# Kernel tuning notes

Measured on AMD Instinct MI355X. Metric: run time of the kernel, lower is better.

Reference implementation:

```python
import jax, jax.numpy as jnp
import numpy as np

NUM_GROUPS = 8
INPUT_DIM = 1024
OUTPUT_DIM = 1024
TOKENS_PER_GROUP = 8192  # rows per group after reshape


def setup_inputs() -> dict:
    key = jax.random.key(0)
    kx, kw = jax.random.split(key)
    # x: [N*G, D_in] as fed to the torch module (it reshapes internally)
    x = jax.random.normal(kx, (TOKENS_PER_GROUP * NUM_GROUPS, INPUT_DIM), dtype=jnp.float32)
    # Stacked per-group Linear weights, torch layout [D_out, D_in] per group.
    # Xavier-normal gain=1: std = sqrt(2 / (fan_in + fan_out))
    std = np.sqrt(2.0 / (INPUT_DIM + OUTPUT_DIM)).astype(np.float32)
    W = jax.random.normal(kw, (NUM_GROUPS, OUTPUT_DIM, INPUT_DIM), dtype=jnp.float32) * std
    return {"x": x, "W": W}


def reference(x, W):
    # x: [N*G, D_in] -> [N, G, D_in]
    n = x.shape[0] // NUM_GROUPS
    xg = x.reshape(n, NUM_GROUPS, INPUT_DIM)
    # per-group linear: out[n,g,k] = sum_d xg[n,g,d] * W[g,k,d]
    out = jnp.einsum("ngd,gkd->ngk", xg, W)
    return out.reshape(-1, OUTPUT_DIM)
```

## Files before the change

### kernel.cpp

```cpp
#include <hip/hip_runtime.h>
#include <hip/hip_bf16.h>


namespace {

constexpr int NG   = 8;
constexpr int DIN  = 1024;
constexpr int DOUT = 1024;
constexpr int BM   = 256;
constexpr int BN   = 256;
constexpr int BK   = 64;
constexpr int NKT  = DIN / BK;
constexpr int ROWB = BK * 2;
constexpr int LDS_TILE  = BM * ROWB;
constexpr int LDS_BYTES = 4 * LDS_TILE;
constexpr int JTN  = DOUT / BN;
constexpr size_t WSB_BYTES = (size_t)NG * JTN * NKT * LDS_TILE;

typedef __attribute__((ext_vector_type(8))) short bf16x8;
typedef __attribute__((ext_vector_type(4))) float f32x4;

__device__ __forceinline__ uint2 pack_bf16x4(f32x4 v) {
  union { __hip_bfloat162 h2[2]; uint2 u; } p;
  p.h2[0] = __float22bfloat162_rn(make_float2(v.x, v.y));
  p.h2[1] = __float22bfloat162_rn(make_float2(v.z, v.w));
  return p.u;
}

__device__ __forceinline__ void glds16(const void* g, void* l) {
  __builtin_amdgcn_global_load_lds(
      (const __attribute__((address_space(1))) unsigned int*)g,
      (__attribute__((address_space(3))) unsigned int*)l, 16, 0, 0);
}

#define FENCE() asm volatile("" ::: "memory")
#define BAR()   do { FENCE(); __builtin_amdgcn_s_barrier(); FENCE(); } while (0)
#define LGKM0() asm volatile("s_waitcnt lgkmcnt(0)" ::: "memory")
#define VM0()   asm volatile("s_waitcnt vmcnt(0)" ::: "memory")
#define MFMA_(a, b, c) __builtin_amdgcn_mfma_f32_16x16x32_bf16((a), (b), (c), 0, 0, 0)

__global__ __launch_bounds__(256)
void cvt_w_kernel(const float* __restrict__ W, char* __restrict__ wsB) {
  const int q    = (int)blockIdx.x * 256 + (int)threadIdx.x;
  const int tile = q >> 13;
  const int q13  = q & 8191;
  const int r    = q13 >> 5;
  const int cp   = q13 & 31;
  const int g    = tile >> 6;
  const int jt   = (tile >> 4) & 3;
  const int kt   = tile & 15;

  const float2 s = *(const float2*)(
      W + ((size_t)(g * DOUT + jt * 256 + r)) * DIN + kt * 64 + 2 * cp);
  union { __hip_bfloat162 h; unsigned u; } pk;
  pk.h = __float22bfloat162_rn(make_float2(s.x, s.y));

  const int swz = (r & 7) << 4;
  const int dstByte = r * 128 + (((cp >> 2) * 16) ^ swz) + (cp & 3) * 4;
  *(unsigned*)(wsB + (size_t)tile * LDS_TILE + dstByte) = pk.u;
}

#define QPHASE(KS, MH, PRE, POST)                                              \
  do {                                                                         \
    const int cx_ = (KS) ? colx1 : colx0;                                      \
    bf16x8 af0 = *(const bf16x8*)(cA + aRow0 + ((MH)*4+0)*2048 + cx_);         \
    bf16x8 af1 = *(const bf16x8*)(cA + aRow0 + ((MH)*4+1)*2048 + cx_);         \
    bf16x8 af2 = *(const bf16x8*)(cA + aRow0 + ((MH)*4+2)*2048 + cx_);         \
    bf16x8 af3 = *(const bf16x8*)(cA + aRow0 + ((MH)*4+3)*2048 + cx_);         \
    PRE                                                                        \
    BAR();                                                                     \
    LGKM0();                                                                   \
    __builtin_amdgcn_sched_barrier(0);                                         \
    __builtin_amdgcn_s_setprio(1);                                             \
    _Pragma("unroll")                                                          \
    for (int n = 0; n < 4; ++n) {                                              \
      acc[(MH)*4+0][n] = MFMA_(af0, bfr[n], acc[(MH)*4+0][n]);                 \
      acc[(MH)*4+1][n] = MFMA_(af1, bfr[n], acc[(MH)*4+1][n]);                 \
      acc[(MH)*4+2][n] = MFMA_(af2, bfr[n], acc[(MH)*4+2][n]);                 \
      acc[(MH)*4+3][n] = MFMA_(af3, bfr[n], acc[(MH)*4+3][n]);                 \
    }                                                                          \
    __builtin_amdgcn_s_setprio(0);                                             \
    POST                                                                       \
    BAR();                                                                     \
  } while (0)

template <bool WSB>
__global__ __launch_bounds__(512, 2)
void grouped_gemm_8p(const float* __restrict__ X,
                     const float* __restrict__ W,
                     const char* __restrict__ wsB,
                     float* __restrict__ O) {
  extern __shared__ char smem[];
  char* const smA = smem;
  char* const smB = smem + 2 * LDS_TILE;

  const int bid = (int)blockIdx.x;
  const int swz = (bid & 7) * 128 + (bid >> 3);
  const int jt = swz & 3;
  const int it = (swz >> 2) & 31;
  const int g  = swz >> 7;

  const int n0 = it * BM;
  const int c0 = jt * BN;

  const int tid  = (int)threadIdx.x;
  const int lane = tid & 63;
  const int wid  = tid >> 6;
  const int wr   = wid >> 2;
  const int wc   = wid & 3;

  const int s_lane = tid & 15;
  const int s_row  = tid >> 4;

  const float* Ag = X + ((size_t)(n0 + s_row) * NG + g) * DIN + s_lane * 4;
  constexpr size_t ASTR = (size_t)32 * NG * DIN;

  const float* Bg = W + (size_t)g * DOUT * DIN + (size_t)(c0 + s_row) * DIN
                      + s_lane * 4;
  constexpr size_t BSTR = (size_t)32 * DIN;

  const char* BgT = wsB + ((size_t)(g * JTN + jt) * NKT) * LDS_TILE;
  const int bOff = tid * 16;

  const int wb0 = s_row * ROWB + ((s_lane * 8) ^ ((s_row & 7) << 4));

  const int fr = lane & 15;
  const int fq = lane >> 4;
  const int swzm  = (fr & 7) << 4;
  const int colx0 = (fq * 16) ^ swzm;
  const int colx1 = (64 + fq * 16) ^ swzm;
  const int aRow0 = (wr * 128 + fr) * ROWB;
  const int bRow0 = (wc * 64  + fr) * ROWB;

  f32x4 aS[8], bS[8];
  f32x4 acc[8][4];
#pragma unroll
  for (int m = 0; m < 8; ++m)
#pragma unroll
    for (int n = 0; n < 4; ++n) acc[m][n] = (f32x4){0.f, 0.f, 0.f, 0.f};

  if (WSB) {
#pragma unroll
    for (int p = 0; p < 4; ++p)
      glds16(BgT + bOff + p * 8192, smB + bOff + p * 8192);
  } else {
#pragma unroll
    for (int p = 0; p < 8; ++p) bS[p] = *(const f32x4*)(Bg + p * BSTR);
  }
#pragma unroll
  for (int p = 0; p < 8; ++p) aS[p] = *(const f32x4*)(Ag + p * ASTR);
#pragma unroll
  for (int p = 0; p < 8; ++p)
    *(uint2*)(smA + wb0 + p * 4096) = pack_bf16x4(aS[p]);
  if (!WSB) {
#pragma unroll
    for (int p = 0; p < 8; ++p)
      *(uint2*)(smB + wb0 + p * 4096) = pack_bf16x4(bS[p]);
  }
  VM0();
  LGKM0();
  BAR();

#pragma unroll 2
  for (int t = 0; t < NKT; ++t) {
    char* const cA = smA + (t & 1) * LDS_TILE;
    char* const cB = smB + (t & 1) * LDS_TILE;
    char* const nA = smA + ((t & 1) ^ 1) * LDS_TILE;
    char* const nB = smB + ((t & 1) ^ 1) * LDS_TILE;
    const bool stage = (t + 1) < NKT;

    bf16x8 bfr[4];
#pragma unroll
    for (int n = 0; n < 4; ++n)
      bfr[n] = *(const bf16x8*)(cB + bRow0 + n * 2048 + colx0);

    QPHASE(0, 0,
      { if (stage) {
          const float* An = Ag + (size_t)(t + 1) * BK;
          _Pragma("unroll")
          for (int p = 0; p < 8; ++p) aS[p] = *(const f32x4*)(An + p * ASTR);
          if (WSB) {
            const char* Bn = BgT + (size_t)(t + 1) * LDS_TILE;
            _Pragma("unroll")
            for (int p = 0; p < 4; ++p)
              glds16(Bn + bOff + p * 8192, nB + bOff + p * 8192);
          }
        } },
      { });

    QPHASE(0, 1,
      { if (!WSB && stage) {
          const float* Bn = Bg + (size_t)(t + 1) * BK;
          _Pragma("unroll")
          for (int p = 0; p < 8; ++p) bS[p] = *(const f32x4*)(Bn + p * BSTR);
        } },
      { });

    QPHASE(1, 0,
      { _Pragma("unroll")
        for (int n = 0; n < 4; ++n)
          bfr[n] = *(const bf16x8*)(cB + bRow0 + n * 2048 + colx1);
      },
      { if (stage) {
          _Pragma("unroll")
          for (int p = 0; p < 8; ++p)
            *(uint2*)(nA + wb0 + p * 4096) = pack_bf16x4(aS[p]);
        } });

    QPHASE(1, 1, { },
      { if (!WSB && stage) {
          _Pragma("unroll")
          for (int p = 0; p < 8; ++p)
            *(uint2*)(nB + wb0 + p * 4096) = pack_bf16x4(bS[p]);
        }
        LGKM0();
        if (WSB && stage) { VM0(); } });
  }

#pragma unroll
  for (int m = 0; m < 8; ++m) {
#pragma unroll
    for (int r = 0; r < 4; ++r) {
      const int row = wr * 128 + m * 16 + fq * 4 + r;
      float* orow = O + ((size_t)(n0 + row) * NG + g) * DOUT + c0 + wc * 64;
#pragma unroll
      for (int n = 0; n < 4; ++n) {
        orow[n * 16 + fr] = acc[m][n][r];
      }
    }
  }
}

}

extern "C" void kernel_launch(void* const* d_in, const int* in_sizes, int n_in,
                              void* d_out, int out_size, void* d_ws, size_t ws_size,
                              hipStream_t stream) {
  (void)n_in; (void)out_size;
  const float* X = (const float*)d_in[0];
  const float* W = (const float*)d_in[1];
  float* O = (float*)d_out;

  const int tokens_total = in_sizes[0] / DIN;
  const int ntok_per_g   = tokens_total / NG;
  const int grid = NG * (ntok_per_g / BM) * (DOUT / BN);

  if (ws_size >= WSB_BYTES) {
    const int cvt_grid = (int)(WSB_BYTES / 4 / 256);
    cvt_w_kernel<<<dim3(cvt_grid), dim3(256), 0, stream>>>(W, (char*)d_ws);
    (void)hipFuncSetAttribute((const void*)grouped_gemm_8p<true>,
                              hipFuncAttributeMaxDynamicSharedMemorySize,
                              LDS_BYTES);
    grouped_gemm_8p<true><<<dim3(grid), dim3(512), LDS_BYTES, stream>>>(
        X, W, (const char*)d_ws, O);
  } else {
    (void)hipFuncSetAttribute((const void*)grouped_gemm_8p<false>,
                              hipFuncAttributeMaxDynamicSharedMemorySize,
                              LDS_BYTES);
    grouped_gemm_8p<false><<<dim3(grid), dim3(512), LDS_BYTES, stream>>>(
        X, W, nullptr, O);
  }
}
```

Measured before the change: 239.1 us.

## Pre-convert X to swizzled bf16 tiles and run a pure async-load GEMM

Adds a pre-pass kernel that converts X from fp32 into bf16 tiles laid out and swizzled exactly as the LDS expects, stored in workspace. A new GEMM kernel then streams both A and B through direct global-to-LDS loads, with no in-kernel fp32 loading or conversion of X. The aim is to halve the A-operand bytes the GEMM reads and to drop conversion work from its main loop. The cost is an extra pass that reads all of X and writes a bf16 copy, plus a larger workspace requirement; the older path is kept as a fallback when the workspace is too small.

```diff
diff --git a/kernel.cpp b/kernel.cpp
--- a/kernel.cpp
+++ b/kernel.cpp
@@ -15,7 +15,10 @@
 constexpr int LDS_TILE  = BM * ROWB;
 constexpr int LDS_BYTES = 4 * LDS_TILE;
 constexpr int JTN  = DOUT / BN;
+constexpr int ITN  = 32;
 constexpr size_t WSB_BYTES = (size_t)NG * JTN * NKT * LDS_TILE;
+constexpr size_t WSA_BYTES = (size_t)NG * ITN * NKT * LDS_TILE;
+constexpr size_t WSF_BYTES = WSA_BYTES + WSB_BYTES;
 
 typedef __attribute__((ext_vector_type(8))) short bf16x8;
 typedef __attribute__((ext_vector_type(4))) float f32x4;
@@ -25,6 +28,15 @@
   p.h2[0] = __float22bfloat162_rn(make_float2(v.x, v.y));
   p.h2[1] = __float22bfloat162_rn(make_float2(v.z, v.w));
   return p.u;
+}
+
+__device__ __forceinline__ bf16x8 pack_bf16x8v(f32x4 lo, f32x4 hi) {
+  union { __hip_bfloat162 h2[4]; bf16x8 v; } p;
+  p.h2[0] = __float22bfloat162_rn(make_float2(lo.x, lo.y));
+  p.h2[1] = __float22bfloat162_rn(make_float2(lo.z, lo.w));
+  p.h2[2] = __float22bfloat162_rn(make_float2(hi.x, hi.y));
+  p.h2[3] = __float22bfloat162_rn(make_float2(hi.z, hi.w));
+  return p.v;
 }
 
 __device__ __forceinline__ void glds16(const void* g, void* l) {
@@ -51,13 +63,31 @@
   const int kt   = tile & 15;
 
   const float2 s = *(const float2*)(
-      W + ((size_t)(g * DOUT + jt * 256 + r)) * DIN + kt * 64 + 2 * cp);
+      W + ((size_t)(g * DOUT + jt * BN + r)) * DIN + kt * 64 + 2 * cp);
   union { __hip_bfloat162 h; unsigned u; } pk;
   pk.h = __float22bfloat162_rn(make_float2(s.x, s.y));
 
   const int swz = (r & 7) << 4;
-  const int dstByte = r * 128 + (((cp >> 2) * 16) ^ swz) + (cp & 3) * 4;
+  const int dstByte = r * ROWB + (((cp >> 2) * 16) ^ swz) + (cp & 3) * 4;
   *(unsigned*)(wsB + (size_t)tile * LDS_TILE + dstByte) = pk.u;
+}
+
+__global__ __launch_bounds__(256)
+void cvt_x_kernel(const float* __restrict__ X, char* __restrict__ wsA) {
+  const int q    = (int)blockIdx.x * 256 + (int)threadIdx.x;
+  const int tile = q >> 11;
+  const int c    = q & 2047;
+  const int r    = c >> 3;
+  const int w    = c & 7;
+  const int g    = tile >> 9;
+  const int it   = (tile >> 4) & 31;
+  const int kt   = tile & 15;
+
+  const float* src = X + ((size_t)(it * BM + r) * NG + g) * DIN
+                       + kt * 64 + (w ^ (r & 7)) * 8;
+  f32x4 lo = *(const f32x4*)(src);
+  f32x4 hi = *(const f32x4*)(src + 4);
+  *(bf16x8*)(wsA + (size_t)q * 16) = pack_bf16x8v(lo, hi);
 }
 
 #define QPHASE(KS, MH, PRE, POST)                                              \
@@ -84,6 +114,106 @@
     BAR();                                                                     \
   } while (0)
 
+__global__ __launch_bounds__(512, 2)
+void gemm_full(const char* __restrict__ wsA, const char* __restrict__ wsB,
+               float* __restrict__ O) {
+  extern __shared__ char smem[];
+  char* const smA = smem;
+  char* const smB = smem + 2 * LDS_TILE;
+
+  const int bid = (int)blockIdx.x;
+  const int swz = (bid & 7) * 128 + (bid >> 3);
+  const int jt = swz & 3;
+  const int it = (swz >> 2) & 31;
+  const int g  = swz >> 7;
+
+  const int n0 = it * BM;
+  const int c0 = jt * BN;
+
+  const int tid  = (int)threadIdx.x;
+  const int lane = tid & 63;
+  const int wid  = tid >> 6;
+  const int wr   = wid >> 2;
+  const int wc   = wid & 3;
+
+  const char* AgT = wsA + (size_t)((g * ITN + it) * NKT) * LDS_TILE;
+  const char* BgT = wsB + (size_t)((g * JTN + jt) * NKT) * LDS_TILE;
+  const int bOff = tid * 16;
+
+  const int fr = lane & 15;
+  const int fq = lane >> 4;
+  const int swzm  = (fr & 7) << 4;
+  const int colx0 = (fq * 16) ^ swzm;
+  const int colx1 = (64 + fq * 16) ^ swzm;
+  const int aRow0 = (wr * 128 + fr) * ROWB;
+  const int bRow0 = (wc * 64  + fr) * ROWB;
+
+  f32x4 acc[8][4];
+#pragma unroll
+  for (int m = 0; m < 8; ++m)
+#pragma unroll
+    for (int n = 0; n < 4; ++n) acc[m][n] = (f32x4){0.f, 0.f, 0.f, 0.f};
+
+#pragma unroll
+  for (int p = 0; p < 4; ++p) {
+    glds16(AgT + bOff + p * 8192, smA + bOff + p * 8192);
+    glds16(BgT + bOff + p * 8192, smB + bOff + p * 8192);
+  }
+  VM0();
+  BAR();
+
+#pragma unroll 2
+  for (int t = 0; t < NKT; ++t) {
+    char* const cA = smA + (t & 1) * LDS_TILE;
+    char* const cB = smB + (t & 1) * LDS_TILE;
+    char* const nA = smA + ((t & 1) ^ 1) * LDS_TILE;
+    char* const nB = smB + ((t & 1) ^ 1) * LDS_TILE;
+    const bool stage = (t + 1) < NKT;
+
+    bf16x8 bfr[4];
+#pragma unroll
+    for (int n = 0; n < 4; ++n)
+      bfr[n] = *(const bf16x8*)(cB + bRow0 + n * 2048 + colx0);
+
+    QPHASE(0, 0,
+      { if (stage) {
+          const char* An = AgT + (size_t)(t + 1) * LDS_TILE;
+          const char* Bn = BgT + (size_t)(t + 1) * LDS_TILE;
+          _Pragma("unroll")
+          for (int p = 0; p < 4; ++p) {
+            glds16(An + bOff + p * 8192, nA + bOff + p * 8192);
+            glds16(Bn + bOff + p * 8192, nB + bOff + p * 8192);
+          }
+        } },
+      { });
+
+    QPHASE(0, 1, { }, { });
+
+    QPHASE(1, 0,
+      { _Pragma("unroll")
+        for (int n = 0; n < 4; ++n)
+          bfr[n] = *(const bf16x8*)(cB + bRow0 + n * 2048 + colx1);
+      },
+      { });
+
+    QPHASE(1, 1, { },
+      { if (stage) { VM0(); } });
+  }
+
+#pragma unroll
+  for (int m = 0; m < 8; ++m) {
+#pragma unroll
+    for (int r = 0; r < 4; ++r) {
+      const int row = wr * 128 + m * 16 + fq * 4 + r;
+      float* orow = O + ((size_t)(n0 + row) * NG + g) * DOUT + c0 + wc * 64;
+#pragma unroll
+      for (int n = 0; n < 4; ++n) {
+        orow[n * 16 + fr] = acc[m][n][r];
+      }
+    }
+  }
+}
+
 template <bool WSB>
 __global__ __launch_bounds__(512, 2)
 void grouped_gemm_8p(const float* __restrict__ X,
@@ -245,9 +375,18 @@
   const int ntok_per_g   = tokens_total / NG;
   const int grid = NG * (ntok_per_g / BM) * (DOUT / BN);
 
-  if (ws_size >= WSB_BYTES) {
-    const int cvt_grid = (int)(WSB_BYTES / 4 / 256);
-    cvt_w_kernel<<<dim3(cvt_grid), dim3(256), 0, stream>>>(W, (char*)d_ws);
+  if (ws_size >= WSF_BYTES) {
+    char* wsA = (char*)d_ws;
+    char* wsB = (char*)d_ws + WSA_BYTES;
+    cvt_x_kernel<<<dim3((int)(WSA_BYTES / 16 / 256)), dim3(256), 0, stream>>>(X, wsA);
+    cvt_w_kernel<<<dim3((int)(WSB_BYTES / 4 / 256)), dim3(256), 0, stream>>>(W, wsB);
+    (void)hipFuncSetAttribute((const void*)gemm_full,
+                              hipFuncAttributeMaxDynamicSharedMemorySize,
+                              LDS_BYTES);
+    gemm_full<<<dim3(grid), dim3(512), LDS_BYTES, stream>>>(wsA, wsB, O);
+  } else if (ws_size >= WSB_BYTES) {
+    cvt_w_kernel<<<dim3((int)(WSB_BYTES / 4 / 256)), dim3(256), 0, stream>>>(
+        W, (char*)d_ws);
     (void)hipFuncSetAttribute((const void*)grouped_gemm_8p<true>,
                               hipFuncAttributeMaxDynamicSharedMemorySize,
                               LDS_BYTES);
```

After: 273.7 us. +14.5%, slower.
